# Optimization experiments

Hardware: AMD Instinct MI355X
Metric: run time of the kernel (lower is better)

Reference implementation:

```python
import jax, jax.numpy as jnp
import numpy as np
import math

NUM_HEADS = 32
NUM_KV_HEADS = 8
HEAD_DIM = 128
HIDDEN = 4096
BATCH = 2
SEQ = 2048
MASK_MIN = -1e9


def _rope(x, cos, sin):
    # x: [B, S, H, D], cos/sin: [S, D/2]
    d2 = x.shape[-1] // 2
    x1, x2 = x[..., :d2], x[..., d2:]
    c = cos[None, :, None, :]
    s = sin[None, :, None, :]
    return jnp.concatenate([x1 * c - x2 * s, x2 * c + x1 * s], axis=-1)


def setup_inputs() -> dict:
    key = jax.random.key(0)
    k1, k2, k3 = jax.random.split(key, 3)
    hidden_states = jax.random.normal(k1, (BATCH, SEQ, HIDDEN), dtype=jnp.float32) * 0.02
    Wqkv = jax.random.normal(k2, (HIDDEN, (NUM_HEADS + 2 * NUM_KV_HEADS) * HEAD_DIM), dtype=jnp.float32) * (HIDDEN ** -0.5)
    Wo = jax.random.normal(k3, (NUM_HEADS * HEAD_DIM, HIDDEN), dtype=jnp.float32) * (HIDDEN ** -0.5)
    pos = np.arange(SEQ, dtype=np.float32)
    inv_freq = 1.0 / (10000.0 ** (np.arange(0, HEAD_DIM, 2, dtype=np.float32) / HEAD_DIM))
    freqs = np.outer(pos, inv_freq)  # [S, D/2]
    cos = jnp.asarray(np.cos(freqs), dtype=jnp.float32)
    sin = jnp.asarray(np.sin(freqs), dtype=jnp.float32)
    # causal additive mask [B, 1, S, S]
    causal = np.triu(np.full((SEQ, SEQ), MASK_MIN, dtype=np.float32), k=1)
    attention_mask = jnp.broadcast_to(jnp.asarray(causal)[None, None], (BATCH, 1, SEQ, SEQ))
    return {"hidden_states": hidden_states, "Wqkv": Wqkv, "Wo": Wo,
            "cos": cos, "sin": sin, "attention_mask": attention_mask}


def reference(hidden_states, Wqkv, Wo, cos, sin, attention_mask):
    B, S, H = hidden_states.shape
    n_rep = NUM_HEADS // NUM_KV_HEADS
    qkv = jnp.einsum('bsh,hd->bsd', hidden_states, Wqkv)
    q_end = NUM_HEADS * HEAD_DIM
    k_end = q_end + NUM_KV_HEADS * HEAD_DIM
    q = qkv[..., :q_end].reshape(B, S, NUM_HEADS, HEAD_DIM)
    k = qkv[..., q_end:k_end].reshape(B, S, NUM_KV_HEADS, HEAD_DIM)
    v = qkv[..., k_end:].reshape(B, S, NUM_KV_HEADS, HEAD_DIM)
    q = _rope(q, cos, sin)
    k = _rope(k, cos, sin)
    # repeat_kv: expand kv heads to query heads
    k = jnp.repeat(k, n_rep, axis=2)  # [B, S, NH, D]
    v = jnp.repeat(v, n_rep, axis=2)
    scores = jnp.einsum('bqhd,bkhd->bhqk', q, k) / math.sqrt(HEAD_DIM)
    scores = scores + attention_mask
    scores = jnp.maximum(scores, jnp.finfo(scores.dtype).min)
    probs = jax.nn.softmax(scores.astype(jnp.float32), axis=-1).astype(q.dtype)
    attn = jnp.einsum('bhqk,bkhd->bqhd', probs, v)  # [B, S, NH, D]
    attn = attn.reshape(B, S, NUM_HEADS * HEAD_DIM)
    return jnp.einsum('bsd,dh->bsh', attn, Wo)
```

## Files before the change

### kernel.cpp

```cpp
#include <hip/hip_runtime.h>

typedef unsigned short u16;
typedef __bf16 bf16x8 __attribute__((ext_vector_type(8)));
typedef float f32x4 __attribute__((ext_vector_type(4)));
typedef float f32x16 __attribute__((ext_vector_type(16)));
typedef u16 u16x4 __attribute__((ext_vector_type(4)));

#define SEQ 2048
#define NQKV 6144
#define HID 4096

__device__ inline u16 f2bf(float f) {
  union { float f; unsigned u; } x; x.f = f;
  unsigned r = x.u + 0x7fffu + ((x.u >> 16) & 1u);
  return (u16)(r >> 16);
}
__device__ inline float bf2f(u16 u) {
  union { unsigned u; float f; } x; x.u = ((unsigned)u) << 16;
  return x.f;
}
__device__ inline f32x4 mfma16(bf16x8 a, bf16x8 b, f32x4 c) {
  return __builtin_amdgcn_mfma_f32_16x16x32_bf16(a, b, c, 0, 0, 0);
}
__device__ inline f32x16 mfma32(bf16x8 a, bf16x8 b, f32x16 c) {
  return __builtin_amdgcn_mfma_f32_32x32x16_bf16(a, b, c, 0, 0, 0);
}
__device__ inline unsigned cvtpk(float lo, float hi) {
  unsigned r;
  asm("v_cvt_pk_bf16_f32 %0, %1, %2" : "=v"(r) : "v"(lo), "v"(hi));
  return r;
}
__device__ inline void gload16(const void* g, void* l) {
  __builtin_amdgcn_global_load_lds((const __attribute__((address_space(1))) void*)g,
                                   (__attribute__((address_space(3))) void*)l,
                                   16, 0, 0);
}

__global__ __launch_bounds__(256) void conv_kernel(const float* __restrict__ in,
                                                   u16* __restrict__ out) {
  int i = (blockIdx.x * 256 + threadIdx.x) * 4;
  float4 v = *(const float4*)(in + i);
  u16x4 o;
  o[0] = f2bf(v.x); o[1] = f2bf(v.y); o[2] = f2bf(v.z); o[3] = f2bf(v.w);
  *(u16x4*)(out + i) = o;
}

__global__ __launch_bounds__(256) void transconv_kernel(const float* __restrict__ in,
                                                        u16* __restrict__ out,
                                                        int R, int C) {
  __shared__ u16 tile[32][33];
  int c0 = blockIdx.x * 32, r0 = blockIdx.y * 32;
  int tx = threadIdx.x & 31, ty = threadIdx.x >> 5;
  for (int i = 0; i < 4; ++i)
    tile[ty + 8 * i][tx] = f2bf(in[(size_t)(r0 + ty + 8 * i) * C + c0 + tx]);
  __syncthreads();
  for (int i = 0; i < 4; ++i)
    out[(size_t)(c0 + ty + 8 * i) * R + r0 + tx] = tile[tx][ty + 8 * i];
}

__global__ __launch_bounds__(512, 2) void gemm32_kernel(const u16* __restrict__ A,
                                                        const u16* __restrict__ Bt,
                                                        u16* __restrict__ C,
                                                        int M, int N, int K, int nby) {
  __shared__ __align__(16) u16 As[3][256 * 32];
  __shared__ __align__(16) u16 Bs[3][384 * 32];
  int nwg = gridDim.x;
  int bid = blockIdx.x;
  int s = (bid & 7) * (nwg >> 3) + (bid >> 3);
  int by = s % nby, bx = s / nby;
  int row0 = by * 256, col0 = bx * 384;
  int tid = threadIdx.x, w = tid >> 6, l = tid & 63;
  int wm = w >> 2, wn = w & 3;
  int l31 = l & 31, lh = l >> 5;
  const u16* Ab = A + (size_t)row0 * K;
  const u16* Bb = Bt + (size_t)col0 * K;
  int nkt = K >> 5;

  f32x16 acc[4][3] = {};

#define STA32(tt, bf)                                                         \
  { _Pragma("unroll")                                                         \
    for (int j = 0; j < 2; ++j) {                                             \
      int cid = j * 512 + tid;                                                \
      int row = cid >> 2, cl = cid & 3;                                       \
      gload16(Ab + (size_t)row * K + (tt) * 32 + ((cl ^ ((row >> 1) & 3)) * 8), \
              &As[bf][cid * 8]);                                              \
    } }
#define STB32(tt, bf)                                                         \
  { _Pragma("unroll")                                                         \
    for (int j = 0; j < 3; ++j) {                                             \
      int cid = j * 512 + tid;                                                \
      int row = cid >> 2, cl = cid & 3;                                       \
      gload16(Bb + (size_t)row * K + (tt) * 32 + ((cl ^ ((row >> 1) & 3)) * 8), \
              &Bs[bf][cid * 8]);                                              \
    } }
#define RA32(bf, im, ks, dst)                                                 \
  { int r = wm * 128 + (im) * 32 + l31;                                       \
    dst = *(const bf16x8*)&As[bf][r * 32 + ((((ks) * 2 + lh) ^ ((r >> 1) & 3)) * 8)]; }
#define RB32(bf, in, ks, dst)                                                 \
  { int r = wn * 96 + (in) * 32 + l31;                                        \
    dst = *(const bf16x8*)&Bs[bf][r * 32 + ((((ks) * 2 + lh) ^ ((r >> 1) & 3)) * 8)]; }

  STA32(0, 0); STB32(0, 0); STA32(1, 1); STB32(1, 1);
  asm volatile("s_waitcnt vmcnt(5)" ::: "memory");
  __builtin_amdgcn_s_barrier();

  int cur = 0;
  for (int t = 0; t < nkt; ++t) {
    int nb = cur + 2; if (nb >= 3) nb -= 3;
    bool pf = (t + 2 < nkt);
    bf16x8 a0, a1, a2, a3, b0, b1, b2;
    RA32(cur, 0, 0, a0); RA32(cur, 1, 0, a1); RA32(cur, 2, 0, a2); RA32(cur, 3, 0, a3);
    RB32(cur, 0, 0, b0); RB32(cur, 1, 0, b1); RB32(cur, 2, 0, b2);
    if (pf) STA32(t + 2, nb);
    __builtin_amdgcn_s_barrier();
    asm volatile("s_waitcnt lgkmcnt(0)" ::: "memory");
    __builtin_amdgcn_s_setprio(1);
    acc[0][0] = mfma32(a0, b0, acc[0][0]); acc[0][1] = mfma32(a0, b1, acc[0][1]);
    acc[0][2] = mfma32(a0, b2, acc[0][2]);
    acc[1][0] = mfma32(a1, b0, acc[1][0]); acc[1][1] = mfma32(a1, b1, acc[1][1]);
    acc[1][2] = mfma32(a1, b2, acc[1][2]);
    acc[2][0] = mfma32(a2, b0, acc[2][0]); acc[2][1] = mfma32(a2, b1, acc[2][1]);
    acc[2][2] = mfma32(a2, b2, acc[2][2]);
    acc[3][0] = mfma32(a3, b0, acc[3][0]); acc[3][1] = mfma32(a3, b1, acc[3][1]);
    acc[3][2] = mfma32(a3, b2, acc[3][2]);
    __builtin_amdgcn_s_setprio(0);
    __builtin_amdgcn_s_barrier();
    RA32(cur, 0, 1, a0); RA32(cur, 1, 1, a1); RA32(cur, 2, 1, a2); RA32(cur, 3, 1, a3);
    RB32(cur, 0, 1, b0); RB32(cur, 1, 1, b1); RB32(cur, 2, 1, b2);
    if (pf) STB32(t + 2, nb);
    __builtin_amdgcn_s_barrier();
    asm volatile("s_waitcnt lgkmcnt(0)" ::: "memory");
    __builtin_amdgcn_s_setprio(1);
    acc[0][0] = mfma32(a0, b0, acc[0][0]); acc[0][1] = mfma32(a0, b1, acc[0][1]);
    acc[0][2] = mfma32(a0, b2, acc[0][2]);
    acc[1][0] = mfma32(a1, b0, acc[1][0]); acc[1][1] = mfma32(a1, b1, acc[1][1]);
    acc[1][2] = mfma32(a1, b2, acc[1][2]);
    acc[2][0] = mfma32(a2, b0, acc[2][0]); acc[2][1] = mfma32(a2, b1, acc[2][1]);
    acc[2][2] = mfma32(a2, b2, acc[2][2]);
    acc[3][0] = mfma32(a3, b0, acc[3][0]); acc[3][1] = mfma32(a3, b1, acc[3][1]);
    acc[3][2] = mfma32(a3, b2, acc[3][2]);
    __builtin_amdgcn_s_setprio(0);
    if (pf)              { asm volatile("s_waitcnt vmcnt(5)" ::: "memory"); }
    else if (t + 1 < nkt){ asm volatile("s_waitcnt vmcnt(0)" ::: "memory"); }
    __builtin_amdgcn_s_barrier();
    cur = cur + 1 == 3 ? 0 : cur + 1;
  }
#undef STA32
#undef STB32
#undef RA32
#undef RB32

#pragma unroll
  for (int im = 0; im < 4; ++im)
#pragma unroll
    for (int in = 0; in < 3; ++in)
#pragma unroll
      for (int reg = 0; reg < 16; ++reg) {
        int row = row0 + wm * 128 + im * 32 + (reg & 3) + 8 * (reg >> 2) + 4 * lh;
        int col = col0 + wn * 96 + in * 32 + l31;
        C[(size_t)row * N + col] = f2bf(acc[im][in][reg]);
      }
}

__device__ inline void store_out(u16* p, float v) { *p = f2bf(v); }
__device__ inline void store_out(float* p, float v) { *p = v; }

template <typename OutT>
__global__ __launch_bounds__(512, 2) void gemm_kernel(const u16* __restrict__ A,
                                                      const u16* __restrict__ Bt,
                                                      OutT* __restrict__ C,
                                                      int M, int N, int K, int nby) {
  __shared__ __align__(16) u16 As[2][2][256 * 32];
  __shared__ __align__(16) u16 Bs[2][2][256 * 32];
  int nwg = gridDim.x;
  int bid = blockIdx.x;
  int s = (bid & 7) * (nwg >> 3) + (bid >> 3);
  int by = s % nby, bx = s / nby;
  int row0 = by * 256, col0 = bx * 256;
  int tid = threadIdx.x, w = tid >> 6, l = tid & 63;
  int wm = w >> 2, wn = w & 3;
  int lo = l & 15, hi = l >> 4;
  int sr = tid >> 2;
  int sc = tid & 3;
  int lc = sc ^ ((tid >> 3) & 3);
  const u16* Ab = A + (size_t)row0 * K;
  const u16* Bb = Bt + (size_t)col0 * K;
  int nkt = K >> 6;

  f32x4 acc[8][4] = {};

#define STA(tt, kh)                                                           \
  { _Pragma("unroll")                                                         \
    for (int j = 0; j < 2; ++j) {                                             \
      int row = j * 128 + sr;                                                 \
      gload16(Ab + (size_t)row * K + (tt) * 64 + (kh) * 32 + lc * 8,          \
              &As[(tt) & 1][kh][row * 32 + sc * 8]);                          \
    } }
#define STB(tt, kh)                                                           \
  { _Pragma("unroll")                                                         \
    for (int j = 0; j < 2; ++j) {                                             \
      int row = j * 128 + sr;                                                 \
      gload16(Bb + (size_t)row * K + (tt) * 64 + (kh) * 32 + lc * 8,          \
              &Bs[(tt) & 1][kh][row * 32 + sc * 8]);                          \
    } }
#define RA(cur, kh, fm, dst)                                                  \
  { int r = wm * 128 + (fm) * 16 + lo;                                        \
    dst = *(const bf16x8*)&As[cur][kh][r * 32 + ((hi ^ ((r >> 1) & 3)) * 8)]; }
#define RB(cur, kh, fn, dst)                                                  \
  { int r = wn * 64 + (fn) * 16 + lo;                                         \
    dst = *(const bf16x8*)&Bs[cur][kh][r * 32 + ((hi ^ ((r >> 1) & 3)) * 8)]; }

  STA(0, 0); STB(0, 0); STA(0, 1); STB(0, 1);
  asm volatile("s_waitcnt vmcnt(4)" ::: "memory");
  __builtin_amdgcn_s_barrier();

  bf16x8 af[4], bfr[4];
  for (int t = 0; t < nkt; ++t) {
    int cur = t & 1;
    bool pf = (t + 1 < nkt);
    RA(cur, 0, 0, af[0]); RA(cur, 0, 1, af[1]); RA(cur, 0, 2, af[2]); RA(cur, 0, 3, af[3]);
    RB(cur, 0, 0, bfr[0]); RB(cur, 0, 1, bfr[1]); RB(cur, 0, 2, bfr[2]); RB(cur, 0, 3, bfr[3]);
    if (pf) STA(t + 1, 0);
    __builtin_amdgcn_s_barrier();
    asm volatile("s_waitcnt lgkmcnt(0)" ::: "memory");
    __builtin_amdgcn_s_setprio(1);
#pragma unroll
    for (int fm = 0; fm < 4; ++fm)
#pragma unroll
      for (int fn = 0; fn < 4; ++fn)
        acc[fm][fn] = mfma16(af[fm], bfr[fn], acc[fm][fn]);
    __builtin_amdgcn_s_setprio(0);
    __builtin_amdgcn_s_barrier();
    RA(cur, 0, 4, af[0]); RA(cur, 0, 5, af[1]); RA(cur, 0, 6, af[2]); RA(cur, 0, 7, af[3]);
    if (pf) STB(t + 1, 0);
    __builtin_amdgcn_s_barrier();
    asm volatile("s_waitcnt lgkmcnt(0)" ::: "memory");
    __builtin_amdgcn_s_setprio(1);
#pragma unroll
    for (int fm = 0; fm < 4; ++fm)
#pragma unroll
      for (int fn = 0; fn < 4; ++fn)
        acc[4 + fm][fn] = mfma16(af[fm], bfr[fn], acc[4 + fm][fn]);
    __builtin_amdgcn_s_setprio(0);
    if (pf) { asm volatile("s_waitcnt vmcnt(4)" ::: "memory"); }
    else    { asm volatile("s_waitcnt vmcnt(0)" ::: "memory"); }
    __builtin_amdgcn_s_barrier();
    RA(cur, 1, 0, af[0]); RA(cur, 1, 1, af[1]); RA(cur, 1, 2, af[2]); RA(cur, 1, 3, af[3]);
    RB(cur, 1, 0, bfr[0]); RB(cur, 1, 1, bfr[1]); RB(cur, 1, 2, bfr[2]); RB(cur, 1, 3, bfr[3]);
    if (pf) STA(t + 1, 1);
    __builtin_amdgcn_s_barrier();
    asm volatile("s_waitcnt lgkmcnt(0)" ::: "memory");
    __builtin_amdgcn_s_setprio(1);
#pragma unroll
    for (int fm = 0; fm < 4; ++fm)
#pragma unroll
      for (int fn = 0; fn < 4; ++fn)
        acc[fm][fn] = mfma16(af[fm], bfr[fn], acc[fm][fn]);
    __builtin_amdgcn_s_setprio(0);
    __builtin_amdgcn_s_barrier();
    RA(cur, 1, 4, af[0]); RA(cur, 1, 5, af[1]); RA(cur, 1, 6, af[2]); RA(cur, 1, 7, af[3]);
    if (pf) STB(t + 1, 1);
    __builtin_amdgcn_s_barrier();
    asm volatile("s_waitcnt lgkmcnt(0)" ::: "memory");
    __builtin_amdgcn_s_setprio(1);
#pragma unroll
    for (int fm = 0; fm < 4; ++fm)
#pragma unroll
      for (int fn = 0; fn < 4; ++fn)
        acc[4 + fm][fn] = mfma16(af[fm], bfr[fn], acc[4 + fm][fn]);
    __builtin_amdgcn_s_setprio(0);
    if (pf) { asm volatile("s_waitcnt vmcnt(4)" ::: "memory"); }
    __builtin_amdgcn_s_barrier();
  }
#undef STA
#undef STB
#undef RA
#undef RB

  for (int fm = 0; fm < 8; ++fm)
    for (int fn = 0; fn < 4; ++fn)
      for (int rr = 0; rr < 4; ++rr) {
        int row = row0 + wm * 128 + fm * 16 + hi * 4 + rr;
        int col = col0 + wn * 64 + fn * 16 + lo;
        store_out(&C[(size_t)row * N + col], acc[fm][fn][rr]);
      }
}

__global__ __launch_bounds__(256) void rope_kernel(u16* __restrict__ qkv,
                                                   const float* __restrict__ cosb,
                                                   const float* __restrict__ sinb) {
  int idx = blockIdx.x * 256 + threadIdx.x;
  int d = idx & 63;
  int head = (idx >> 6) % 40;
  int m = idx / (64 * 40);
  int s = m & (SEQ - 1);
  int col = head < 32 ? head * 128 : 4096 + (head - 32) * 128;
  u16* p = qkv + (size_t)m * NQKV + col;
  float x1 = bf2f(p[d]), x2 = bf2f(p[d + 64]);
  float c = cosb[s * 64 + d], sn = sinb[s * 64 + d];
  p[d] = f2bf(x1 * c - x2 * sn);
  p[d + 64] = f2bf(x2 * c + x1 * sn);
}

__global__ __launch_bounds__(256) void vtrans_kernel(const u16* __restrict__ qkv,
                                                     u16* __restrict__ Vt) {
  __shared__ u16 tile[32][33];
  int bid = blockIdx.x;
  int dt = bid & 3;
  int st = (bid >> 2) & 63;
  int bk = bid >> 8;
  int b = bk >> 3, kvh = bk & 7;
  int tx = threadIdx.x & 31, ty = threadIdx.x >> 5;
  for (int i = 0; i < 4; ++i) {
    int s = st * 32 + ty + 8 * i;
    tile[ty + 8 * i][tx] = qkv[(size_t)(b * SEQ + s) * NQKV + 5120 + kvh * 128 + dt * 32 + tx];
  }
  __syncthreads();
  for (int i = 0; i < 4; ++i) {
    int d = dt * 32 + ty + 8 * i;
    Vt[((size_t)bk * 128 + d) * SEQ + st * 32 + tx] = tile[tx][ty + 8 * i];
  }
}

__global__ __launch_bounds__(256, 2) void flash_kernel(const u16* __restrict__ qkv,
                                                       const u16* __restrict__ Vt,
                                                       u16* __restrict__ attn) {
  const float C2 = 0.12751740f;
  int bid = blockIdx.x;
  int bh = bid & 63;
  int pr = bid >> 6;
  int h = bh & 31;
  int b = bh >> 5;
  int w = threadIdx.x >> 6, l = threadIdx.x & 63;
  int hv = l >> 5;
  int q32 = l & 31;
  int kvh = h >> 2;

  __shared__ __align__(16) u16 Ks[2][64 * 128];
  __shared__ __align__(16) u16 Vs[2][128 * 64];

  const u16* kb = qkv + (size_t)(b * SEQ) * NQKV + 4096 + kvh * 128;
  const u16* vtb = Vt + (size_t)(b * 8 + kvh) * 128 * SEQ;

#define STAGEKV(TT, BF)                                                       \
  { _Pragma("unroll")                                                         \
    for (int i = 0; i < 4; ++i) {                                             \
      int ck = w * 4 + i;                                                     \
      int rk = ck * 4 + (l >> 4);                                             \
      gload16(kb + (size_t)((TT) * 64 + rk) * NQKV + (((l & 15) ^ (rk & 7)) * 8), \
              &Ks[BF][ck * 512]);                                             \
      int rv = ck * 8 + (l >> 3);                                             \
      gload16(vtb + (size_t)rv * SEQ + (TT) * 64 + (((l & 7) ^ (rv & 7)) * 8), \
              &Vs[BF][ck * 512]);                                             \
    } }

  for (int pass = 0; pass < 2; ++pass) {
    int qc = pass ? 15 - pr : pr;
    int q0 = qc * 128 + w * 32;
    int qg = q0 + q32;
    __syncthreads();

    bf16x8 qf[8];
    {
      const u16* qr = qkv + (size_t)(b * SEQ + qg) * NQKV + h * 128 + hv * 8;
#pragma unroll
      for (int d0 = 0; d0 < 8; ++d0) qf[d0] = *(const bf16x8*)(qr + d0 * 16);
    }
    f32x16 o[4] = {};
    float mreg = -1e30f, lreg = 0.f;
    int ktend = 2 * qc + 1;
    int mykt = 2 * qc + (w >> 1);

    STAGEKV(0, 0);
    for (int kt = 0; kt <= ktend; ++kt) {
      int buf = kt & 1;
      if (kt < ktend) {
        STAGEKV(kt + 1, buf ^ 1);
        asm volatile("s_waitcnt vmcnt(8)" ::: "memory");
      } else {
        asm volatile("s_waitcnt vmcnt(0)" ::: "memory");
      }
      __builtin_amdgcn_s_barrier();

      if (kt <= mykt) {
        f32x16 s0 = {}, s1 = {};
        int swzk = q32 & 7;
#pragma unroll
        for (int d0 = 0; d0 < 8; ++d0) {
          int sl = (((d0 * 2 + hv) ^ swzk) * 8);
          bf16x8 k0 = *(const bf16x8*)&Ks[buf][q32 * 128 + sl];
          bf16x8 k1 = *(const bf16x8*)&Ks[buf][(32 + q32) * 128 + sl];
          s0 = mfma32(k0, qf[d0], s0);
          s1 = mfma32(k1, qf[d0], s1);
        }
        if (kt == mykt) {
#pragma unroll
          for (int r = 0; r < 16; ++r) {
            int kloc = (r & 3) + 8 * (r >> 2) + 4 * hv;
            if (kt * 64 + kloc > qg) s0[r] = -1e30f;
            if (kt * 64 + 32 + kloc > qg) s1[r] = -1e30f;
          }
        }
        float pm = -1e30f;
#pragma unroll
        for (int r = 0; r < 16; ++r) {
          pm = fmaxf(pm, s0[r]);
          pm = fmaxf(pm, s1[r]);
        }
        pm = fmaxf(pm, __shfl_xor(pm, 32));
        if (!__all(pm - mreg <= 62.746f)) {
          float mnew = fmaxf(mreg, pm);
          float al = exp2f((mreg - mnew) * C2);
          lreg *= al;
#pragma unroll
          for (int r = 0; r < 16; ++r) {
            o[0][r] *= al; o[1][r] *= al; o[2][r] *= al; o[3][r] *= al;
          }
          mreg = mnew;
        }
        float rs = 0.f;
#pragma unroll
        for (int r = 0; r < 16; ++r) {
          s0[r] = exp2f((s0[r] - mreg) * C2); rs += s0[r];
          s1[r] = exp2f((s1[r] - mreg) * C2); rs += s1[r];
        }
        rs += __shfl_xor(rs, 32);
        lreg += rs;
        bf16x8 pa[4];
#define MKPA(KSI, SP, RB)                                                     \
        { unsigned wA = cvtpk(SP[(RB) + 0], SP[(RB) + 1]);                    \
          unsigned wB = cvtpk(SP[(RB) + 2], SP[(RB) + 3]);                    \
          unsigned wC = cvtpk(SP[(RB) + 4], SP[(RB) + 5]);                    \
          unsigned wD = cvtpk(SP[(RB) + 6], SP[(RB) + 7]);                    \
          unsigned sA = __shfl_xor(wA, 32), sB = __shfl_xor(wB, 32);          \
          unsigned sC = __shfl_xor(wC, 32), sD = __shfl_xor(wD, 32);          \
          union { unsigned u[4]; bf16x8 v; } pk;                              \
          pk.u[0] = hv ? sC : wA; pk.u[1] = hv ? sD : wB;                     \
          pk.u[2] = hv ? wC : sA; pk.u[3] = hv ? wD : sB;                     \
          pa[KSI] = pk.v; }
        MKPA(0, s0, 0) MKPA(1, s0, 8) MKPA(2, s1, 0) MKPA(3, s1, 8)
#undef MKPA
#pragma unroll
        for (int db = 0; db < 4; ++db) {
          int rv = db * 32 + q32;
          int swz = rv & 7;
#pragma unroll
          for (int ks = 0; ks < 4; ++ks) {
            bf16x8 vf = *(const bf16x8*)&Vs[buf][rv * 64 + (((ks * 2 + hv) ^ swz) * 8)];
            o[db] = mfma32(vf, pa[ks], o[db]);
          }
        }
      }
    }
    float invl = 1.0f / lreg;
    u16* op = attn + (size_t)(b * SEQ + qg) * 4096 + h * 128 + hv * 4;
#pragma unroll
    for (int db = 0; db < 4; ++db)
#pragma unroll
      for (int g = 0; g < 4; ++g) {
        unsigned w0 = cvtpk(o[db][g * 4 + 0] * invl, o[db][g * 4 + 1] * invl);
        unsigned w1 = cvtpk(o[db][g * 4 + 2] * invl, o[db][g * 4 + 3] * invl);
        uint2 val; val.x = w0; val.y = w1;
        *(uint2*)(op + db * 32 + g * 8) = val;
      }
  }
#undef STAGEKV
}

extern "C" void kernel_launch(void* const* d_in, const int* in_sizes, int n_in,
                              void* d_out, int out_size, void* d_ws, size_t ws_size,
                              hipStream_t stream) {
  const float* hidden = (const float*)d_in[0];
  const float* Wqkv = (const float*)d_in[1];
  const float* Wo = (const float*)d_in[2];
  const float* cosb = (const float*)d_in[3];
  const float* sinb = (const float*)d_in[4];
  float* out = (float*)d_out;

  char* ws = (char*)d_ws;
  u16* R1 = (u16*)ws;
  u16* R2 = (u16*)(ws + 50331648);
  u16* R3 = (u16*)(ws + 100663296);

  conv_kernel<<<16384, 256, 0, stream>>>(hidden, R3);
  transconv_kernel<<<dim3(6144 / 32, 4096 / 32), 256, 0, stream>>>(Wqkv, R1, 4096, 6144);
  gemm32_kernel<<<256, 512, 0, stream>>>(R3, R1, R2, 4096, 6144, 4096, 16);
  rope_kernel<<<40960, 256, 0, stream>>>(R2, cosb, sinb);
  vtrans_kernel<<<4096, 256, 0, stream>>>(R2, R3);
  flash_kernel<<<512, 256, 0, stream>>>(R2, R3, R1);
  transconv_kernel<<<dim3(4096 / 32, 4096 / 32), 256, 0, stream>>>(Wo, R2, 4096, 4096);
  gemm_kernel<float><<<256, 512, 0, stream>>>(R1, R2, out, 4096, 4096, 4096, 16);
}
```

Baseline: 518.2 us.

## Pre-tile QKV GEMM operands into LDS-ready blocked layout during conversion

```diff
diff --git a/kernel.cpp b/kernel.cpp
--- a/kernel.cpp
+++ b/kernel.cpp
@@ -36,13 +36,36 @@
                                    16, 0, 0);
 }
 
+
 __global__ __launch_bounds__(256) void conv_kernel(const float* __restrict__ in,
                                                    u16* __restrict__ out) {
   int i = (blockIdx.x * 256 + threadIdx.x) * 4;
+  int m = i >> 12, k = i & 4095;
   float4 v = *(const float4*)(in + i);
   u16x4 o;
   o[0] = f2bf(v.x); o[1] = f2bf(v.y); o[2] = f2bf(v.z); o[3] = f2bf(v.w);
-  *(u16x4*)(out + i) = o;
+  int p = m >> 8, r = m & 255;
+  int t = k >> 5, kc = (k >> 3) & 3, e = k & 7;
+  int slot = ((r >> 5) << 7) + (kc << 5) + (r & 31);
+  *(u16x4*)(out + ((size_t)(p * 128 + t) * 1024 + slot) * 8 + e) = o;
+}
+
+__global__ __launch_bounds__(256) void transconv_qkv_kernel(const float* __restrict__ in,
+                                                            u16* __restrict__ out) {
+  __shared__ u16 tile[32][33];
+  int c0 = blockIdx.x * 32, r0 = blockIdx.y * 32;
+  int tx = threadIdx.x & 31, ty = threadIdx.x >> 5;
+  for (int i = 0; i < 4; ++i)
+    tile[ty + 8 * i][tx] = f2bf(in[(size_t)(r0 + ty + 8 * i) * NQKV + c0 + tx]);
+  __syncthreads();
+  int t = r0 >> 5;
+  for (int i = 0; i < 4; ++i) {
+    int n = c0 + ty + 8 * i;
+    int p = n / 384, pc = n - p * 384;
+    int kc = tx >> 3, e = tx & 7;
+    int slot = ((pc >> 5) << 7) + (kc << 5) + (pc & 31);
+    out[((size_t)(p * 128 + t) * 1536 + slot) * 8 + e] = tile[tx][ty + 8 * i];
+  }
 }
 
 __global__ __launch_bounds__(256) void transconv_kernel(const float* __restrict__ in,
@@ -58,8 +81,8 @@
     out[(size_t)(c0 + ty + 8 * i) * R + r0 + tx] = tile[tx][ty + 8 * i];
 }
 
-__global__ __launch_bounds__(512, 2) void gemm32_kernel(const u16* __restrict__ A,
-                                                        const u16* __restrict__ Bt,
+__global__ __launch_bounds__(512, 2) void gemm32_kernel(const u16* __restrict__ At,
+                                                        const u16* __restrict__ Btl,
                                                         u16* __restrict__ C,
                                                         int M, int N, int K, int nby) {
   __shared__ __align__(16) u16 As[3][256 * 32];
@@ -72,8 +95,8 @@
   int tid = threadIdx.x, w = tid >> 6, l = tid & 63;
   int wm = w >> 2, wn = w & 3;
   int l31 = l & 31, lh = l >> 5;
-  const u16* Ab = A + (size_t)row0 * K;
-  const u16* Bb = Bt + (size_t)col0 * K;
+  const u16* Ap = At + (size_t)by * 128 * 1024 * 8;
+  const u16* Bp = Btl + (size_t)bx * 128 * 1536 * 8;
   int nkt = K >> 5;
 
   f32x16 acc[4][3] = {};
@@ -82,24 +105,20 @@
   { _Pragma("unroll")                                                         \
     for (int j = 0; j < 2; ++j) {                                             \
       int cid = j * 512 + tid;                                                \
-      int row = cid >> 2, cl = cid & 3;                                       \
-      gload16(Ab + (size_t)row * K + (tt) * 32 + ((cl ^ ((row >> 1) & 3)) * 8), \
-              &As[bf][cid * 8]);                                              \
+      gload16(Ap + ((size_t)(tt) * 1024 + cid) * 8, &As[bf][cid * 8]);        \
     } }
 #define STB32(tt, bf)                                                         \
   { _Pragma("unroll")                                                         \
     for (int j = 0; j < 3; ++j) {                                             \
       int cid = j * 512 + tid;                                                \
-      int row = cid >> 2, cl = cid & 3;                                       \
-      gload16(Bb + (size_t)row * K + (tt) * 32 + ((cl ^ ((row >> 1) & 3)) * 8), \
-              &Bs[bf][cid * 8]);                                              \
+      gload16(Bp + ((size_t)(tt) * 1536 + cid) * 8, &Bs[bf][cid * 8]);        \
     } }
 #define RA32(bf, im, ks, dst)                                                 \
-  { int r = wm * 128 + (im) * 32 + l31;                                       \
-    dst = *(const bf16x8*)&As[bf][r * 32 + ((((ks) * 2 + lh) ^ ((r >> 1) & 3)) * 8)]; }
+  { int slot = ((wm * 4 + (im)) << 7) + (((ks) * 2 + lh) << 5) + l31;         \
+    dst = *(const bf16x8*)&As[bf][slot * 8]; }
 #define RB32(bf, in, ks, dst)                                                 \
-  { int r = wn * 96 + (in) * 32 + l31;                                        \
-    dst = *(const bf16x8*)&Bs[bf][r * 32 + ((((ks) * 2 + lh) ^ ((r >> 1) & 3)) * 8)]; }
+  { int slot = ((wn * 3 + (in)) << 7) + (((ks) * 2 + lh) << 5) + l31;         \
+    dst = *(const bf16x8*)&Bs[bf][slot * 8]; }
 
   STA32(0, 0); STB32(0, 0); STA32(1, 1); STB32(1, 1);
   asm volatile("s_waitcnt vmcnt(5)" ::: "memory");
@@ -484,7 +503,7 @@
   u16* R3 = (u16*)(ws + 100663296);
 
   conv_kernel<<<16384, 256, 0, stream>>>(hidden, R3);
-  transconv_kernel<<<dim3(6144 / 32, 4096 / 32), 256, 0, stream>>>(Wqkv, R1, 4096, 6144);
+  transconv_qkv_kernel<<<dim3(6144 / 32, 4096 / 32), 256, 0, stream>>>(Wqkv, R1);
   gemm32_kernel<<<256, 512, 0, stream>>>(R3, R1, R2, 4096, 6144, 4096, 16);
   rope_kernel<<<40960, 256, 0, stream>>>(R2, cosb, sinb);
   vtrans_kernel<<<4096, 256, 0, stream>>>(R2, R3);
```

Result: no change. 521.1 us (+0.6%).
